# Optimization experiments

Hardware: AMD Instinct MI355X
Metric: run time of the kernel (lower is better)

Reference implementation:

```python
import jax, jax.numpy as jnp
import numpy as np

EMBED = 2048
HEADS = 16
B, T = 4, 2048


def setup_inputs() -> dict:
    key = jax.random.key(0)
    ks = jax.random.split(key, 8)
    s = 1.0 / np.sqrt(EMBED)
    return {
        "k": jax.random.normal(ks[0], (B, T, EMBED), dtype=jnp.float32),
        "q": jax.random.normal(ks[1], (B, T, EMBED), dtype=jnp.float32),
        "v": jax.random.normal(ks[2], (B, T, EMBED), dtype=jnp.float32),
        "Wk": jax.random.uniform(ks[3], (EMBED, EMBED), jnp.float32, -s, s),
        "Wq": jax.random.uniform(ks[4], (EMBED, EMBED), jnp.float32, -s, s),
        "Wv": jax.random.uniform(ks[5], (EMBED, EMBED), jnp.float32, -s, s),
        "Wo": jax.random.uniform(ks[6], (EMBED, EMBED), jnp.float32, -s, s),
        "bo": jax.random.uniform(ks[7], (EMBED,), jnp.float32, -s, s),
    }


def _split_heads(x):
    b, t, e = x.shape
    # 'b t (h n) -> b h t n'
    return x.reshape(b, t, HEADS, e // HEADS).transpose(0, 2, 1, 3)


def reference(k, q, v, Wk, Wq, Wv, Wo, bo):
    keys = _split_heads(k @ Wk.T)      # [b,h,t,n]
    queries = _split_heads(q @ Wq.T)
    values = _split_heads(v @ Wv.T)
    head_dim = queries.shape[-1]
    scale = 1.0 / jnp.sqrt(jnp.asarray(head_dim, queries.dtype))
    att = jnp.einsum('bhqn,bhkn->bhqk', queries, keys) * scale
    att = jax.nn.softmax(att, axis=-1)
    out = jnp.einsum('bhqk,bhkn->bhqn', att, values)  # [b,h,t,n]
    b, h, t, n = out.shape
    out = out.transpose(0, 2, 1, 3).reshape(b, t, h * n)  # 'b h t n -> b t (h n)'
    return out @ Wo.T + bo
```

## Files before the change

### kernel.cpp

```cpp
#include <hip/hip_runtime.h>


typedef __attribute__((ext_vector_type(4))) float f32x4;
typedef __attribute__((ext_vector_type(2))) float f32x2;
typedef __attribute__((ext_vector_type(8))) __bf16 bf16x8;
typedef __attribute__((ext_vector_type(4))) unsigned int u32x4;
typedef __attribute__((ext_vector_type(2))) unsigned int u32x2;

#define DEVI static __device__ __forceinline__

DEVI unsigned short f2bf(float f) {
  union { float f; unsigned u; } x; x.f = f;
  unsigned u = x.u;
  return (unsigned short)((u + 0x7fffu + ((u >> 16) & 1u)) >> 16);
}
DEVI unsigned int pack2(float lo, float hi) {
  return (unsigned int)f2bf(lo) | ((unsigned int)f2bf(hi) << 16);
}
DEVI u32x4 pack8(const f32x4 a, const f32x4 b) {
  u32x4 r;
  r[0] = pack2(a[0], a[1]); r[1] = pack2(a[2], a[3]);
  r[2] = pack2(b[0], b[1]); r[3] = pack2(b[2], b[3]);
  return r;
}
DEVI void gload16(const unsigned short* g, unsigned short* l) {
  __builtin_amdgcn_global_load_lds(
      (const __attribute__((address_space(1))) unsigned int*)g,
      (__attribute__((address_space(3))) unsigned int*)l, 16, 0, 0);
}

template <int CTRL> DEVI float dppf(float x) {
  return __builtin_bit_cast(float, __builtin_amdgcn_update_dpp(
      __builtin_bit_cast(int, x), __builtin_bit_cast(int, x), CTRL, 0xF, 0xF, true));
}
DEVI float rowmax16(float x) {
  x = fmaxf(x, dppf<0x121>(x));
  x = fmaxf(x, dppf<0x122>(x));
  x = fmaxf(x, dppf<0x124>(x));
  x = fmaxf(x, dppf<0x128>(x));
  return x;
}
DEVI float rowsum16(float x) {
  x += dppf<0x121>(x);
  x += dppf<0x122>(x);
  x += dppf<0x124>(x);
  x += dppf<0x128>(x);
  return x;
}

__global__ __launch_bounds__(256) void convA(
    const float* __restrict__ q, const float* __restrict__ k,
    const float* __restrict__ v, unsigned short* __restrict__ dst)
{
  const int z = blockIdx.z;
  const float* src = z == 0 ? q : (z == 1 ? k : v);
  unsigned short* d = dst + (size_t)z * 16777216;
  size_t i = ((size_t)blockIdx.x * 256 + threadIdx.x) * 8;
  f32x4 a = *(const f32x4*)(src + i);
  f32x4 b = *(const f32x4*)(src + i + 4);
  *(u32x4*)(d + i) = pack8(a, b);
}

__global__ __launch_bounds__(256) void convW(
    const float* __restrict__ w0, const float* __restrict__ w1,
    const float* __restrict__ w2, const float* __restrict__ w3,
    unsigned short* __restrict__ dst)
{
  const int z = blockIdx.z;
  const float* src = z == 0 ? w0 : (z == 1 ? w1 : (z == 2 ? w2 : w3));
  unsigned short* d = dst + (size_t)z * 4194304;
  size_t i = ((size_t)blockIdx.x * 256 + threadIdx.x) * 8;
  f32x4 a = *(const f32x4*)(src + i);
  f32x4 b = *(const f32x4*)(src + i + 4);
  *(u32x4*)(d + i) = pack8(a, b);
}

#define STG2(gp, lp, tile) do { \
    gload16((gp) + (size_t)(tile) * 64,            (lp)); \
    gload16((gp) + (size_t)(tile) * 64 + 8 * 2048, (lp) + 8 * 64); \
  } while (0)
#define LDA8(bufoff, ksbit) { \
    _Pragma("unroll") for (int m = 0; m < 8; m++) \
      a[m] = *(const bf16x8*)(As + (bufoff) + (aoff[m] ^ (ksbit))); }
#define LDB2(bufoff, ksbit, n0) { \
    b0 = *(const bf16x8*)(Bs + (bufoff) + (boff[n0] ^ (ksbit))); \
    b1 = *(const bf16x8*)(Bs + (bufoff) + (boff[(n0) + 1] ^ (ksbit))); }
#define MM2(n0) { \
    __builtin_amdgcn_s_setprio(1); \
    _Pragma("unroll") for (int m = 0; m < 8; m++) { \
      acc[m][n0] = __builtin_amdgcn_mfma_f32_16x16x32_bf16(a[m], b0, acc[m][n0], 0, 0, 0); \
      acc[m][(n0) + 1] = __builtin_amdgcn_mfma_f32_16x16x32_bf16(a[m], b1, acc[m][(n0) + 1], 0, 0, 0); \
    } \
    __builtin_amdgcn_s_setprio(0); }
#define BARX() { __builtin_amdgcn_sched_barrier(0); __builtin_amdgcn_s_barrier(); }
#define WVM(n) asm volatile("s_waitcnt vmcnt(" #n ")" ::: "memory");

DEVI void gemm256_bf16(const unsigned short* __restrict__ A,
                       const unsigned short* __restrict__ Bm,
                       unsigned short* As, unsigned short* Bs,
                       int bm, int bn, int tid, f32x4 (&acc)[8][4])
{
  const int lane = tid & 63, w = tid >> 6;
  const int wm = w >> 2, wn = w & 3;
  const int sr = lane >> 3;
  const int sc = (lane & 7) ^ sr;
  const unsigned short* gA0 = A  + (size_t)(bm * 256 +   0 + w * 16 + sr) * 2048 + sc * 8;
  const unsigned short* gA1 = A  + (size_t)(bm * 256 + 128 + w * 16 + sr) * 2048 + sc * 8;
  const unsigned short* gB0 = Bm + (size_t)(bn * 256 +   0 + w * 16 + sr) * 2048 + sc * 8;
  const unsigned short* gB1 = Bm + (size_t)(bn * 256 + 128 + w * 16 + sr) * 2048 + sc * 8;
  unsigned short* lA00 = As +         (  0 + w * 16) * 64;
  unsigned short* lA01 = As +         (128 + w * 16) * 64;
  unsigned short* lA10 = As + 16384 + (  0 + w * 16) * 64;
  unsigned short* lA11 = As + 16384 + (128 + w * 16) * 64;
  unsigned short* lB00 = Bs +         (  0 + w * 16) * 64;
  unsigned short* lB01 = Bs +         (128 + w * 16) * 64;
  unsigned short* lB10 = Bs + 16384 + (  0 + w * 16) * 64;
  unsigned short* lB11 = Bs + 16384 + (128 + w * 16) * 64;

  const int fr = lane & 15, fk = lane >> 4;
  const int swz = (fk ^ (lane & 7)) << 3;
  int aoff[8], boff[4];
#pragma unroll
  for (int m = 0; m < 8; m++) aoff[m] = (wm * 128 + m * 16 + fr) * 64 + swz;
#pragma unroll
  for (int n = 0; n < 4; n++) boff[n] = (wn * 64 + n * 16 + fr) * 64 + swz;

  bf16x8 a[8], b0, b1;

  STG2(gA0, lA00, 0); STG2(gA1, lA01, 0); STG2(gB0, lB00, 0); STG2(gB1, lB01, 0);
  STG2(gA0, lA10, 1);
  WVM(2) BARX()

  for (int t = 0; t < 30; t += 2) {
    LDA8(0, 0) LDB2(0, 0, 0) STG2(gA1, lA11, t + 1);
    BARX() MM2(0) BARX()
    LDB2(0, 0, 2) STG2(gB0, lB10, t + 1);
    BARX() MM2(2) BARX()
    LDA8(0, 32) LDB2(0, 32, 0) STG2(gB1, lB11, t + 1);
    BARX() MM2(0) BARX()
    LDB2(0, 32, 2) STG2(gA0, lA00, t + 2);
    BARX() MM2(2) WVM(2) BARX()
    LDA8(16384, 0) LDB2(16384, 0, 0) STG2(gA1, lA01, t + 2);
    BARX() MM2(0) BARX()
    LDB2(16384, 0, 2) STG2(gB0, lB00, t + 2);
    BARX() MM2(2) BARX()
    LDA8(16384, 32) LDB2(16384, 32, 0) STG2(gB1, lB01, t + 2);
    BARX() MM2(0) BARX()
    LDB2(16384, 32, 2) STG2(gA0, lA10, t + 3);
    BARX() MM2(2) WVM(2) BARX()
  }
  LDA8(0, 0) LDB2(0, 0, 0) STG2(gA1, lA11, 31);
  BARX() MM2(0) BARX()
  LDB2(0, 0, 2) STG2(gB0, lB10, 31);
  BARX() MM2(2) BARX()
  LDA8(0, 32) LDB2(0, 32, 0) STG2(gB1, lB11, 31);
  BARX() MM2(0) BARX()
  LDB2(0, 32, 2)
  BARX() MM2(2) WVM(0) BARX()
  LDA8(16384, 0) LDB2(16384, 0, 0)
  BARX() MM2(0) BARX()
  LDB2(16384, 0, 2)
  BARX() MM2(2) BARX()
  LDA8(16384, 32) LDB2(16384, 32, 0)
  BARX() MM2(0) BARX()
  LDB2(16384, 32, 2)
  BARX() MM2(2)
}

DEVI int xcd_swz256(int bid) { return ((bid & 7) << 5) | (bid >> 3); }

__global__ __launch_bounds__(512, 2) void qkv_gemm_bf(
    const unsigned short* __restrict__ Abf, const unsigned short* __restrict__ Wbf,
    unsigned short* __restrict__ O0, unsigned short* __restrict__ O1,
    unsigned short* __restrict__ O2)
{
  __shared__ unsigned short As[2 * 256 * 64];
  __shared__ unsigned short Bs[2 * 256 * 64];
  const int z = blockIdx.z;
  const unsigned short* A = Abf + (size_t)z * 16777216;
  const unsigned short* W = Wbf + (size_t)z * 4194304;
  unsigned short* O = z == 0 ? O0 : (z == 1 ? O1 : O2);

  const int tid = threadIdx.x;
  const int lane = tid & 63, w = tid >> 6;
  const int wm = w >> 2, wn = w & 3;
  const int bs = xcd_swz256(blockIdx.x);
  const int bm = bs >> 3, bn = bs & 7;

  f32x4 acc[8][4];
#pragma unroll
  for (int m = 0; m < 8; m++)
#pragma unroll
    for (int n = 0; n < 4; n++) acc[m][n] = (f32x4)(0.0f);

  gemm256_bf16(A, W, As, Bs, bm, bn, tid, acc);

  if (z == 2) {
#pragma unroll
    for (int m = 0; m < 8; m++) {
      int rowg = bm * 256 + wm * 128 + m * 16 + (lane >> 4) * 4;
      int bb = rowg >> 11, t0 = rowg & 2047;
#pragma unroll
      for (int n = 0; n < 4; n++) {
        int col = bn * 256 + wn * 64 + n * 16 + (lane & 15);
        int hh = col >> 7, dd = col & 127;
        u32x2 wv;
        wv[0] = pack2(acc[m][n][0], acc[m][n][1]);
        wv[1] = pack2(acc[m][n][2], acc[m][n][3]);
        *(u32x2*)(O + (((size_t)(bb * 16 + hh) * 128 + dd) << 11) + t0) = wv;
      }
    }
    return;
  }

  const bool evenlane = (lane & 1) == 0;
#pragma unroll
  for (int m = 0; m < 8; m++) {
    int rowg = bm * 256 + wm * 128 + m * 16 + (lane >> 4) * 4;
#pragma unroll
    for (int n = 0; n < 4; n += 2) {
#pragma unroll
      for (int j = 0; j < 4; j++) {
        float v0 = acc[m][n][j], v1 = acc[m][n + 1][j];
        float p0 = __shfl_xor(v0, 1);
        float p1 = __shfl_xor(v1, 1);
        int row = rowg + j;
        int b = row >> 11, t = row & 2047;
        int colbase = bn * 256 + wn * 64;
        int col = evenlane ? (colbase + n * 16 + (lane & 15))
                           : (colbase + (n + 1) * 16 + (lane & 15) - 1);
        unsigned int wv = evenlane ? pack2(v0, p0) : pack2(p1, v1);
        int h = col >> 7, d = col & 127;
        *(unsigned int*)(O + (((size_t)(b * 16 + h) * 2048 + t) << 7) + d) = wv;
      }
    }
  }
}

__global__ __launch_bounds__(512, 2) void out_gemm_bf(
    const unsigned short* __restrict__ Ab, const unsigned short* __restrict__ Wb,
    const float* __restrict__ bias, float* __restrict__ Out)
{
  __shared__ unsigned short As[2 * 256 * 64];
  __shared__ unsigned short Bs[2 * 256 * 64];
  const int tid = threadIdx.x;
  const int lane = tid & 63, w = tid >> 6;
  const int wm = w >> 2, wn = w & 3;
  const int bs = xcd_swz256(blockIdx.x);
  const int bm = bs >> 3, bn = bs & 7;

  f32x4 acc[8][4];
#pragma unroll
  for (int m = 0; m < 8; m++)
#pragma unroll
    for (int n = 0; n < 4; n++) acc[m][n] = (f32x4)(0.0f);

  gemm256_bf16(Ab, Wb, As, Bs, bm, bn, tid, acc);

  float bv[4];
#pragma unroll
  for (int n = 0; n < 4; n++) bv[n] = bias[bn * 256 + wn * 64 + n * 16 + (lane & 15)];
  const bool evenlane = (lane & 1) == 0;
#pragma unroll
  for (int m = 0; m < 8; m++) {
    int rowg = bm * 256 + wm * 128 + m * 16 + (lane >> 4) * 4;
#pragma unroll
    for (int n = 0; n < 4; n += 2) {
#pragma unroll
      for (int j = 0; j < 4; j++) {
        float v0 = acc[m][n][j] + bv[n];
        float v1 = acc[m][n + 1][j] + bv[n + 1];
        float p0 = __shfl_xor(v0, 1);
        float p1 = __shfl_xor(v1, 1);
        int row = rowg + j;
        int colbase = bn * 256 + wn * 64;
        int col = evenlane ? (colbase + n * 16 + (lane & 15))
                           : (colbase + (n + 1) * 16 + (lane & 15) - 1);
        f32x2 wv;
        if (evenlane) { wv[0] = v0; wv[1] = p0; }
        else          { wv[0] = p1; wv[1] = v1; }
        *(f32x2*)(Out + (size_t)row * 2048 + col) = wv;
      }
    }
  }
}

__global__ __launch_bounds__(256) void qkv_gemm(
    const float* __restrict__ A0, const float* __restrict__ A1, const float* __restrict__ A2,
    const float* __restrict__ W0, const float* __restrict__ W1, const float* __restrict__ W2,
    unsigned short* __restrict__ O0, unsigned short* __restrict__ O1, unsigned short* __restrict__ O2)
{
  __shared__ unsigned short As[128 * 32];
  __shared__ unsigned short Bs[128 * 32];
  const int z = blockIdx.z;
  const float* A = z == 0 ? A0 : (z == 1 ? A1 : A2);
  const float* W = z == 0 ? W0 : (z == 1 ? W1 : W2);
  unsigned short* O = z == 0 ? O0 : (z == 1 ? O1 : O2);

  const int tid = threadIdx.x;
  const int lane = tid & 63;
  const int wave = tid >> 6;
  const int wm = wave >> 1, wn = wave & 1;
  const int bm = blockIdx.x >> 4, bn = blockIdx.x & 15;

  const int srow = tid >> 1;
  const int shalf = tid & 1;
  const float* Ap = A + (size_t)(bm * 128 + srow) * 2048 + shalf * 16;
  const float* Wp = W + (size_t)(bn * 128 + srow) * 2048 + shalf * 16;
  const int ssw = (srow >> 1) & 3;
  const int aoff0 = srow * 32 + (((shalf * 2 + 0) ^ ssw) << 3);
  const int aoff1 = srow * 32 + (((shalf * 2 + 1) ^ ssw) << 3);

  const int frow = lane & 15;
  const int fk = lane >> 4;

  f32x4 acc[4][4];
#pragma unroll
  for (int m = 0; m < 4; m++)
#pragma unroll
    for (int n = 0; n < 4; n++) acc[m][n] = (f32x4)(0.0f);

  for (int kk = 0; kk < 2048; kk += 32) {
    f32x4 a0 = *(const f32x4*)(Ap + kk);
    f32x4 a1 = *(const f32x4*)(Ap + kk + 4);
    f32x4 a2 = *(const f32x4*)(Ap + kk + 8);
    f32x4 a3 = *(const f32x4*)(Ap + kk + 12);
    f32x4 b0 = *(const f32x4*)(Wp + kk);
    f32x4 b1 = *(const f32x4*)(Wp + kk + 4);
    f32x4 b2 = *(const f32x4*)(Wp + kk + 8);
    f32x4 b3 = *(const f32x4*)(Wp + kk + 12);
    __syncthreads();
    *(u32x4*)(As + aoff0) = pack8(a0, a1);
    *(u32x4*)(As + aoff1) = pack8(a2, a3);
    *(u32x4*)(Bs + aoff0) = pack8(b0, b1);
    *(u32x4*)(Bs + aoff1) = pack8(b2, b3);
    __syncthreads();
    bf16x8 af[4], bfr[4];
#pragma unroll
    for (int m = 0; m < 4; m++) {
      int r = wm * 64 + m * 16 + frow;
      af[m] = *(const bf16x8*)(As + r * 32 + ((fk ^ ((r >> 1) & 3)) << 3));
    }
#pragma unroll
    for (int n = 0; n < 4; n++) {
      int r = wn * 64 + n * 16 + frow;
      bfr[n] = *(const bf16x8*)(Bs + r * 32 + ((fk ^ ((r >> 1) & 3)) << 3));
    }
#pragma unroll
    for (int m = 0; m < 4; m++)
#pragma unroll
      for (int n = 0; n < 4; n++)
        acc[m][n] = __builtin_amdgcn_mfma_f32_16x16x32_bf16(af[m], bfr[n], acc[m][n], 0, 0, 0);
  }

  if (z == 2) {
#pragma unroll
    for (int m = 0; m < 4; m++) {
      int rowg = bm * 128 + wm * 64 + m * 16 + (lane >> 4) * 4;
      int bb = rowg >> 11, t0 = rowg & 2047;
#pragma unroll
      for (int n = 0; n < 4; n++) {
        int col = bn * 128 + wn * 64 + n * 16 + (lane & 15);
        int hh = col >> 7, dd = col & 127;
        u32x2 wv;
        wv[0] = pack2(acc[m][n][0], acc[m][n][1]);
        wv[1] = pack2(acc[m][n][2], acc[m][n][3]);
        *(u32x2*)(O + (((size_t)(bb * 16 + hh) * 128 + dd) << 11) + t0) = wv;
      }
    }
    return;
  }

  const bool evenlane = (lane & 1) == 0;
#pragma unroll
  for (int m = 0; m < 4; m++) {
    int rowg = bm * 128 + wm * 64 + m * 16 + (lane >> 4) * 4;
#pragma unroll
    for (int n = 0; n < 4; n += 2) {
#pragma unroll
      for (int j = 0; j < 4; j++) {
        float v0 = acc[m][n][j], v1 = acc[m][n + 1][j];
        float p0 = __shfl_xor(v0, 1);
        float p1 = __shfl_xor(v1, 1);
        int row = rowg + j;
        int b = row >> 11, t = row & 2047;
        int colbase = bn * 128 + wn * 64;
        int col = evenlane ? (colbase + n * 16 + (lane & 15))
                           : (colbase + (n + 1) * 16 + (lane & 15) - 1);
        unsigned int wv = evenlane ? pack2(v0, p0) : pack2(p1, v1);
        int h = col >> 7, d = col & 127;
        *(unsigned int*)(O + (((size_t)(b * 16 + h) * 2048 + t) << 7) + d) = wv;
      }
    }
  }
}

__global__ __launch_bounds__(256, 2) void attn(
    const unsigned short* __restrict__ Qw, const unsigned short* __restrict__ Kw,
    const unsigned short* __restrict__ VwT, unsigned short* __restrict__ attout)
{
  __shared__ unsigned short Ks[2][64 * 128];
  __shared__ unsigned short Vs[2][128 * 64];
  __shared__ unsigned short Ps[128 * 64];

  const int bid = blockIdx.x;
  const int work = ((bid & 7) << 7) | (bid >> 3);
  const int bh = work >> 4;
  const int qtile = work & 15;
  const int b = bh >> 4, h = bh & 15;
  const unsigned short* Qbase = Qw + (size_t)bh * 2048 * 128 + qtile * 128 * 128;
  const unsigned short* Kbase = Kw + (size_t)bh * 2048 * 128;
  const unsigned short* VbaseT = VwT + (size_t)bh * 2048 * 128;
  const int tid = threadIdx.x, lane = tid & 63, w = tid >> 6;
  const int frow = lane & 15, fk = lane >> 4;

  bf16x8 qf[2][4];
#pragma unroll
  for (int m = 0; m < 2; m++)
#pragma unroll
    for (int ks = 0; ks < 4; ks++)
      qf[m][ks] = *(const bf16x8*)(Qbase + (size_t)(w * 32 + m * 16 + frow) * 128 + ks * 32 + fk * 8);

  const int krow_i = lane >> 4;
  const int kslot = lane & 15;
  const int vrow_i = lane >> 3;
  const int vslot = (lane & 7) ^ vrow_i;

  f32x4 o[2][8];
#pragma unroll
  for (int m = 0; m < 2; m++)
#pragma unroll
    for (int n = 0; n < 8; n++) o[m][n] = (f32x4)(0.0f);
  float m_r[2][4], l_r[2][4];
#pragma unroll
  for (int m = 0; m < 2; m++)
#pragma unroll
    for (int j = 0; j < 4; j++) { m_r[m][j] = -INFINITY; l_r[m][j] = 0.f; }
  const float SC = 0.12751721769f;
  const float THR = 90.5f;

  {
#pragma unroll
    for (int i = 0; i < 4; i++) {
      int row = w * 16 + i * 4 + krow_i;
      gload16(Kbase + (size_t)row * 128 + ((kslot ^ (row & 15)) << 3),
              &Ks[0][(w * 16 + i * 4) * 128]);
    }
#pragma unroll
    for (int i = 0; i < 4; i++) {
      int d = w * 32 + i * 8 + vrow_i;
      gload16(VbaseT + (size_t)d * 2048 + vslot * 8,
              &Vs[0][(w * 32 + i * 8) * 64]);
    }
  }

  for (int kt = 0; kt < 32; kt++) {
    const int cur = kt & 1;
    __syncthreads();

    const bool have_next = (kt + 1) < 32;
    if (have_next) {
      const unsigned short* Kt = Kbase + (kt + 1) * 64 * 128;
#pragma unroll
      for (int i = 0; i < 4; i++) {
        int row = w * 16 + i * 4 + krow_i;
        gload16(Kt + (size_t)row * 128 + ((kslot ^ (row & 15)) << 3),
                &Ks[cur ^ 1][(w * 16 + i * 4) * 128]);
      }
#pragma unroll
      for (int i = 0; i < 4; i++) {
        int d = w * 32 + i * 8 + vrow_i;
        gload16(VbaseT + (size_t)d * 2048 + (kt + 1) * 64 + vslot * 8,
                &Vs[cur ^ 1][(w * 32 + i * 8) * 64]);
      }
    }

    f32x4 s[2][4];
#pragma unroll
    for (int m = 0; m < 2; m++)
#pragma unroll
      for (int n = 0; n < 4; n++) s[m][n] = (f32x4)(0.0f);
    __builtin_amdgcn_s_setprio(1);
#pragma unroll
    for (int ks = 0; ks < 4; ks++) {
#pragma unroll
      for (int n = 0; n < 4; n++) {
        int brow = n * 16 + frow;
        bf16x8 bk = *(const bf16x8*)(&Ks[cur][0] + brow * 128 + (((ks * 4 + fk) ^ (brow & 15)) << 3));
#pragma unroll
        for (int m = 0; m < 2; m++)
          s[m][n] = __builtin_amdgcn_mfma_f32_16x16x32_bf16(qf[m][ks], bk, s[m][n], 0, 0, 0);
      }
    }
    __builtin_amdgcn_s_setprio(0);

#pragma unroll
    for (int m = 0; m < 2; m++) {
#pragma unroll
      for (int j = 0; j < 4; j++) {
        float mx = fmaxf(fmaxf(s[m][0][j], s[m][1][j]), fmaxf(s[m][2][j], s[m][3][j]));
        mx = rowmax16(mx);
        float mo = m_r[m][j];
        if (!__all(mx - mo <= THR)) {
          float mnew = fmaxf(mo, mx);
          float f = __builtin_amdgcn_exp2f((mo - mnew) * SC);
          m_r[m][j] = mnew;
          l_r[m][j] *= f;
#pragma unroll
          for (int n = 0; n < 8; n++) o[m][n][j] *= f;
        }
        float mm = m_r[m][j];
        float psum = 0.f;
#pragma unroll
        for (int n = 0; n < 4; n++) {
          float p = __builtin_amdgcn_exp2f((s[m][n][j] - mm) * SC);
          s[m][n][j] = p;
          psum += p;
        }
        l_r[m][j] += rowsum16(psum);

        int row = w * 32 + m * 16 + (lane >> 4) * 4 + j;
        int swzp = row & 7;
        unsigned prv[4];
#pragma unroll
        for (int n = 0; n < 4; n++) {
          float p = s[m][n][j];
          float ph = dppf<0xB1>(p);
          unsigned pr;
          asm("v_cvt_pk_bf16_f32 %0, %1, %2" : "=v"(pr) : "v"(p), "v"(ph));
          prv[n] = pr;
        }
        if (!(lane & 1)) {
#pragma unroll
          for (int n = 0; n < 4; n++) {
            int col = frow + 16 * n;
            *(unsigned*)((char*)Ps + row * 128 + (((col >> 3) ^ swzp) << 4) + (col & 7) * 2) = prv[n];
          }
        }
      }
    }

    __builtin_amdgcn_s_setprio(1);
#pragma unroll
    for (int ks = 0; ks < 2; ks++) {
      bf16x8 ap[2];
#pragma unroll
      for (int m = 0; m < 2; m++) {
        int arow = w * 32 + m * 16 + frow;
        ap[m] = *(const bf16x8*)((char*)Ps + arow * 128 + (((ks * 4 + fk) ^ (arow & 7)) << 4));
      }
#pragma unroll
      for (int n = 0; n < 8; n++) {
        int vrow = n * 16 + frow;
        bf16x8 bv = *(const bf16x8*)((char*)&Vs[cur][0] + vrow * 128 + (((ks * 4 + fk) ^ (vrow & 7)) << 4));
#pragma unroll
        for (int m = 0; m < 2; m++)
          o[m][n] = __builtin_amdgcn_mfma_f32_16x16x32_bf16(ap[m], bv, o[m][n], 0, 0, 0);
      }
    }
    __builtin_amdgcn_s_setprio(0);
  }

  const bool evenlane = (lane & 1) == 0;
#pragma unroll
  for (int m = 0; m < 2; m++) {
    float inv[4];
#pragma unroll
    for (int j = 0; j < 4; j++) inv[j] = 1.0f / l_r[m][j];
#pragma unroll
    for (int n = 0; n < 8; n += 2) {
#pragma unroll
      for (int j = 0; j < 4; j++) {
        float v0 = o[m][n][j] * inv[j], v1 = o[m][n + 1][j] * inv[j];
        float p0 = __shfl_xor(v0, 1);
        float p1 = __shfl_xor(v1, 1);
        int tq = qtile * 128 + w * 32 + m * 16 + (lane >> 4) * 4 + j;
        int col = evenlane ? (n * 16 + (lane & 15)) : ((n + 1) * 16 + (lane & 15) - 1);
        unsigned int wv = evenlane ? pack2(v0, p0) : pack2(p1, v1);
        *(unsigned int*)(attout + (size_t)(b * 2048 + tq) * 2048 + h * 128 + col) = wv;
      }
    }
  }
}

__global__ __launch_bounds__(256) void out_gemm(
    const unsigned short* __restrict__ Ab, const float* __restrict__ W,
    const float* __restrict__ bias, float* __restrict__ Out)
{
  __shared__ unsigned short As[128 * 32];
  __shared__ unsigned short Bs[128 * 32];

  const int tid = threadIdx.x;
  const int lane = tid & 63;
  const int wave = tid >> 6;
  const int wm = wave >> 1, wn = wave & 1;
  const int bm = blockIdx.x >> 4, bn = blockIdx.x & 15;

  const int srow = tid >> 1;
  const int shalf = tid & 1;
  const unsigned short* Ap = Ab + (size_t)(bm * 128 + srow) * 2048 + shalf * 16;
  const float* Wp = W + (size_t)(bn * 128 + srow) * 2048 + shalf * 16;
  const int ssw = (srow >> 1) & 3;
  const int aoff0 = srow * 32 + (((shalf * 2 + 0) ^ ssw) << 3);
  const int aoff1 = srow * 32 + (((shalf * 2 + 1) ^ ssw) << 3);

  const int frow = lane & 15;
  const int fk = lane >> 4;

  f32x4 acc[4][4];
#pragma unroll
  for (int m = 0; m < 4; m++)
#pragma unroll
    for (int n = 0; n < 4; n++) acc[m][n] = (f32x4)(0.0f);

  for (int kk = 0; kk < 2048; kk += 32) {
    u32x4 a0 = *(const u32x4*)(Ap + kk);
    u32x4 a1 = *(const u32x4*)(Ap + kk + 8);
    f32x4 b0 = *(const f32x4*)(Wp + kk);
    f32x4 b1 = *(const f32x4*)(Wp + kk + 4);
    f32x4 b2 = *(const f32x4*)(Wp + kk + 8);
    f32x4 b3 = *(const f32x4*)(Wp + kk + 12);
    __syncthreads();
    *(u32x4*)(As + aoff0) = a0;
    *(u32x4*)(As + aoff1) = a1;
    *(u32x4*)(Bs + aoff0) = pack8(b0, b1);
    *(u32x4*)(Bs + aoff1) = pack8(b2, b3);
    __syncthreads();
    bf16x8 af[4], bfr[4];
#pragma unroll
    for (int m = 0; m < 4; m++) {
      int r = wm * 64 + m * 16 + frow;
      af[m] = *(const bf16x8*)(As + r * 32 + ((fk ^ ((r >> 1) & 3)) << 3));
    }
#pragma unroll
    for (int n = 0; n < 4; n++) {
      int r = wn * 64 + n * 16 + frow;
      bfr[n] = *(const bf16x8*)(Bs + r * 32 + ((fk ^ ((r >> 1) & 3)) << 3));
    }
#pragma unroll
    for (int m = 0; m < 4; m++)
#pragma unroll
      for (int n = 0; n < 4; n++)
        acc[m][n] = __builtin_amdgcn_mfma_f32_16x16x32_bf16(af[m], bfr[n], acc[m][n], 0, 0, 0);
  }

  float bv[4];
#pragma unroll
  for (int n = 0; n < 4; n++) bv[n] = bias[bn * 128 + wn * 64 + n * 16 + (lane & 15)];
  const bool evenlane = (lane & 1) == 0;
#pragma unroll
  for (int m = 0; m < 4; m++) {
    int rowg = bm * 128 + wm * 64 + m * 16 + (lane >> 4) * 4;
#pragma unroll
    for (int n = 0; n < 4; n += 2) {
#pragma unroll
      for (int j = 0; j < 4; j++) {
        float v0 = acc[m][n][j] + bv[n];
        float v1 = acc[m][n + 1][j] + bv[n + 1];
        float p0 = __shfl_xor(v0, 1);
        float p1 = __shfl_xor(v1, 1);
        int row = rowg + j;
        int colbase = bn * 128 + wn * 64;
        int col = evenlane ? (colbase + n * 16 + (lane & 15))
                           : (colbase + (n + 1) * 16 + (lane & 15) - 1);
        f32x2 wv;
        if (evenlane) { wv[0] = v0; wv[1] = p0; }
        else          { wv[0] = p1; wv[1] = v1; }
        *(f32x2*)(Out + (size_t)row * 2048 + col) = wv;
      }
    }
  }
}

extern "C" void kernel_launch(void* const* d_in, const int* in_sizes, int n_in,
                              void* d_out, int out_size, void* d_ws, size_t ws_size,
                              hipStream_t stream)
{
  const float* k  = (const float*)d_in[0];
  const float* q  = (const float*)d_in[1];
  const float* v  = (const float*)d_in[2];
  const float* Wk = (const float*)d_in[3];
  const float* Wq = (const float*)d_in[4];
  const float* Wv = (const float*)d_in[5];
  const float* Wo = (const float*)d_in[6];
  const float* bo = (const float*)d_in[7];
  float* out = (float*)d_out;

  const size_t HSZ = (size_t)4 * 16 * 2048 * 128;

  if (ws_size >= (size_t)224 << 20) {
    unsigned short* Abf = (unsigned short*)d_ws;
    unsigned short* Wbf = Abf + 3 * HSZ;
    unsigned short* Qw  = Wbf + 4 * 4194304;
    unsigned short* Kw  = Qw + HSZ;
    unsigned short* Vw  = Kw + HSZ;
    unsigned short* Aw  = Abf;

    convA<<<dim3(8192, 1, 3), 256, 0, stream>>>(q, k, v, Abf);
    convW<<<dim3(2048, 1, 4), 256, 0, stream>>>(Wq, Wk, Wv, Wo, Wbf);
    qkv_gemm_bf<<<dim3(256, 1, 3), 512, 0, stream>>>(Abf, Wbf, Qw, Kw, Vw);
    attn<<<dim3(1024), 256, 0, stream>>>(Qw, Kw, Vw, Aw);
    out_gemm_bf<<<dim3(256), 512, 0, stream>>>(Aw, Wbf + 3 * 4194304, bo, out);
  } else {
    unsigned short* Qw = (unsigned short*)d_ws;
    unsigned short* Kw = Qw + HSZ;
    unsigned short* Vw = Kw + HSZ;
    unsigned short* Aw = Vw + HSZ;
    qkv_gemm<<<dim3(1024, 1, 3), 256, 0, stream>>>(q, k, v, Wq, Wk, Wv, Qw, Kw, Vw);
    attn<<<dim3(1024), 256, 0, stream>>>(Qw, Kw, Vw, Aw);
    out_gemm<<<dim3(1024), 256, 0, stream>>>(Aw, Wo, bo, out);
  }
}
```

Baseline: 556.0 us.

## Fold softmax scale into Q, defer row-sum reduction, lazy rowmax in attention

Pre-multiplies Q by the softmax scale (times log2 e) during conversion and in the projection epilogue, so the attention inner loop computes exp2(s - m) without a multiply. The per-tile cross-lane rowsum is replaced by per-lane partial sums that are reduced once at the end. The rowmax DPP reduction now runs only when the lazy-rescale threshold is exceeded, and the first QK MFMA takes a zero accumulator instead of separately zero-initialised registers. The aim is fewer VALU and DPP operations per key tile in the softmax. The trade-off is that Q is scaled before bf16 rounding, which slightly changes numerics.

```diff
diff --git a/kernel.cpp b/kernel.cpp
--- a/kernel.cpp
+++ b/kernel.cpp
@@ -8,6 +8,8 @@
 typedef __attribute__((ext_vector_type(2))) unsigned int u32x2;
 
 #define DEVI static __device__ __forceinline__
+
+#define SCQ 0.12751721769f
 
 DEVI unsigned short f2bf(float f) {
   union { float f; unsigned u; } x; x.f = f;
@@ -54,10 +56,11 @@
 {
   const int z = blockIdx.z;
   const float* src = z == 0 ? q : (z == 1 ? k : v);
+  const float scl = z == 0 ? SCQ : 1.0f;
   unsigned short* d = dst + (size_t)z * 16777216;
   size_t i = ((size_t)blockIdx.x * 256 + threadIdx.x) * 8;
-  f32x4 a = *(const f32x4*)(src + i);
-  f32x4 b = *(const f32x4*)(src + i + 4);
+  f32x4 a = *(const f32x4*)(src + i) * scl;
+  f32x4 b = *(const f32x4*)(src + i + 4) * scl;
   *(u32x4*)(d + i) = pack8(a, b);
 }
 
@@ -371,6 +374,7 @@
     return;
   }
 
+  const float scl = (z == 0) ? SCQ : 1.0f;
   const bool evenlane = (lane & 1) == 0;
 #pragma unroll
   for (int m = 0; m < 4; m++) {
@@ -379,7 +383,7 @@
     for (int n = 0; n < 4; n += 2) {
 #pragma unroll
       for (int j = 0; j < 4; j++) {
-        float v0 = acc[m][n][j], v1 = acc[m][n + 1][j];
+        float v0 = acc[m][n][j] * scl, v1 = acc[m][n + 1][j] * scl;
         float p0 = __shfl_xor(v0, 1);
         float p1 = __shfl_xor(v1, 1);
         int row = rowg + j;
@@ -431,13 +435,12 @@
   for (int m = 0; m < 2; m++)
 #pragma unroll
     for (int n = 0; n < 8; n++) o[m][n] = (f32x4)(0.0f);
-  float m_r[2][4], l_r[2][4];
+  float m_r[2][4], l_p[2][4];
 #pragma unroll
   for (int m = 0; m < 2; m++)
 #pragma unroll
-    for (int j = 0; j < 4; j++) { m_r[m][j] = -INFINITY; l_r[m][j] = 0.f; }
-  const float SC = 0.12751721769f;
-  const float THR = 90.5f;
+    for (int j = 0; j < 4; j++) { m_r[m][j] = -INFINITY; l_p[m][j] = 0.f; }
+  const float THRL = 11.5f;
 
   {
 #pragma unroll
@@ -476,13 +479,17 @@
     }
 
     f32x4 s[2][4];
-#pragma unroll
-    for (int m = 0; m < 2; m++)
-#pragma unroll
-      for (int n = 0; n < 4; n++) s[m][n] = (f32x4)(0.0f);
     __builtin_amdgcn_s_setprio(1);
 #pragma unroll
-    for (int ks = 0; ks < 4; ks++) {
+    for (int n = 0; n < 4; n++) {
+      int brow = n * 16 + frow;
+      bf16x8 bk = *(const bf16x8*)(&Ks[cur][0] + brow * 128 + ((fk ^ (brow & 15)) << 3));
+#pragma unroll
+      for (int m = 0; m < 2; m++)
+        s[m][n] = __builtin_amdgcn_mfma_f32_16x16x32_bf16(qf[m][0], bk, (f32x4)(0.0f), 0, 0, 0);
+    }
+#pragma unroll
+    for (int ks = 1; ks < 4; ks++) {
 #pragma unroll
       for (int n = 0; n < 4; n++) {
         int brow = n * 16 + frow;
@@ -499,25 +506,24 @@
 #pragma unroll
       for (int j = 0; j < 4; j++) {
         float mx = fmaxf(fmaxf(s[m][0][j], s[m][1][j]), fmaxf(s[m][2][j], s[m][3][j]));
-        mx = rowmax16(mx);
         float mo = m_r[m][j];
-        if (!__all(mx - mo <= THR)) {
-          float mnew = fmaxf(mo, mx);
-          float f = __builtin_amdgcn_exp2f((mo - mnew) * SC);
+        if (!__all(mx - mo <= THRL)) {
+          float mnew = fmaxf(mo, rowmax16(mx));
+          float f = __builtin_amdgcn_exp2f(mo - mnew);
           m_r[m][j] = mnew;
-          l_r[m][j] *= f;
+          l_p[m][j] *= f;
 #pragma unroll
           for (int n = 0; n < 8; n++) o[m][n][j] *= f;
         }
         float mm = m_r[m][j];
-        float psum = 0.f;
+        float ps = 0.f;
 #pragma unroll
         for (int n = 0; n < 4; n++) {
-          float p = __builtin_amdgcn_exp2f((s[m][n][j] - mm) * SC);
+          float p = __builtin_amdgcn_exp2f(s[m][n][j] - mm);
           s[m][n][j] = p;
-          psum += p;
+          ps += p;
         }
-        l_r[m][j] += rowsum16(psum);
+        l_p[m][j] += ps;
 
         int row = w * 32 + m * 16 + (lane >> 4) * 4 + j;
         int swzp = row & 7;
@@ -566,7 +572,7 @@
   for (int m = 0; m < 2; m++) {
     float inv[4];
 #pragma unroll
-    for (int j = 0; j < 4; j++) inv[j] = 1.0f / l_r[m][j];
+    for (int j = 0; j < 4; j++) inv[j] = 1.0f / rowsum16(l_p[m][j]);
 #pragma unroll
     for (int n = 0; n < 8; n += 2) {
 #pragma unroll
```

Measured after the change: 524.8 us. 5.6% less time.
